# Performance work log

Measured on AMD Instinct MI355X. Metric: run time of the kernel, lower is better.

The kernel has to match this reference:

```python
import jax, jax.numpy as jnp
import numpy as np

B = 4096
N_FEAT = 4
VOCAB = 100000
EMB = 64
N_NEG = 3
TEMP = 1.0
EPS = 1e-8  # torch.cosine_similarity eps


def setup_inputs() -> dict:
    key = jax.random.key(0)
    ks = jax.random.split(key, 12)
    inp = {}
    inp['user_ids'] = jax.random.randint(ks[0], (B, N_FEAT), 0, VOCAB)
    inp['item_ids'] = jax.random.randint(ks[1], (B, N_FEAT), 0, VOCAB)
    inp['sw_ids'] = jax.random.randint(ks[2], (B,), 0, VOCAB)
    inp['user_tables'] = jax.random.normal(ks[3], (N_FEAT, VOCAB, EMB), jnp.float32) * 0.05
    inp['item_tables'] = jax.random.normal(ks[4], (N_FEAT, VOCAB, EMB), jnp.float32) * 0.05
    # sample weights must be positive (log is taken)
    inp['sw_table'] = jax.random.uniform(ks[5], (VOCAB,), jnp.float32) * 0.99 + 0.01
    inp['uW1'] = jax.random.normal(ks[6], (256, 256), jnp.float32) * 0.05
    inp['ub1'] = jnp.zeros((256,), jnp.float32)
    inp['uW2'] = jax.random.normal(ks[7], (256, 128), jnp.float32) * 0.05
    inp['ub2'] = jnp.zeros((128,), jnp.float32)
    inp['iW1'] = jax.random.normal(ks[8], (256, 256), jnp.float32) * 0.05
    inp['ib1'] = jnp.zeros((256,), jnp.float32)
    inp['iW2'] = jax.random.normal(ks[9], (256, 128), jnp.float32) * 0.05
    inp['ib2'] = jnp.zeros((128,), jnp.float32)
    return inp


def _embed(tables, ids):
    # tables: [F, V, E], ids: [B, F] -> [B, F*E]
    e = jax.vmap(lambda tbl, idx: tbl[idx], in_axes=(0, 1))(tables, ids)  # [F, B, E]
    return jnp.transpose(e, (1, 0, 2)).reshape(ids.shape[0], -1)


def _mlp(x, W1, b1, W2, b2):
    # torch-rechub MLP with output_layer=False: activation after every layer
    h = jax.nn.relu(x @ W1 + b1)
    return jax.nn.relu(h @ W2 + b2)


def reference(user_ids, item_ids, sw_ids, user_tables, item_tables, sw_table,
              uW1, ub1, uW2, ub2, iW1, ib1, iW2, ib2):
    u = _mlp(_embed(user_tables, user_ids), uW1, ub1, uW2, ub2)   # [B, 128]
    v = _mlp(_embed(item_tables, item_ids), iW1, ib1, iW2, ib2)   # [B, 128]
    un = u / jnp.maximum(jnp.linalg.norm(u, axis=-1, keepdims=True), EPS)
    vn = v / jnp.maximum(jnp.linalg.norm(v, axis=-1, keepdims=True), EPS)
    pred = un @ vn.T                                              # [B, B] cosine sim
    sw = sw_table[sw_ids]                                         # [B]
    scores = pred - jnp.log(sw)[None, :]                          # debias per item column
    # in-batch negative sampling: row i pairs with cols (i..i+n_neg) mod B
    rows = jnp.repeat(jnp.arange(B), N_NEG + 1)
    cols = ((jnp.arange(B)[:, None] + jnp.arange(N_NEG + 1)[None, :]) % B).reshape(-1)
    out = scores[rows, cols] / TEMP
    return out.reshape(B, N_NEG + 1)
```

## Files before the change

### kernel.cpp

```cpp
#include <hip/hip_runtime.h>
#include <math.h>

#define BATCH 4096
#define NFEAT 4
#define VOCAB 100000
#define EMB 64
#define D_IN 256
#define D_H 256
#define D_O 128
#define ROWS 16
#define XS_STRIDE 264
#define YS_STRIDE 132

typedef __attribute__((ext_vector_type(8))) short bf16x8;
typedef __attribute__((ext_vector_type(4))) float f32x4;

__device__ inline ushort f2bf(float f) {
  union { float f; unsigned u; } v; v.f = f;
  unsigned u = v.u;
  return (ushort)((u + 0x7fffu + ((u >> 16) & 1u)) >> 16);
}

__global__ __launch_bounds__(256) void prep_kernel(
    const float* __restrict__ uW1, const float* __restrict__ uW2,
    const float* __restrict__ iW1, const float* __restrict__ iW2,
    ushort* __restrict__ W1tu, ushort* __restrict__ W2tu,
    ushort* __restrict__ W1ti, ushort* __restrict__ W2ti) {
  int idx = blockIdx.x * 256 + threadIdx.x;
  if (idx < 65536) {
    int n = idx >> 8, k = idx & 255;
    W1tu[idx] = f2bf(uW1[k * 256 + n]);
  } else if (idx < 131072) {
    int j = idx - 65536; int n = j >> 8, k = j & 255;
    W1ti[j] = f2bf(iW1[k * 256 + n]);
  } else if (idx < 163840) {
    int j = idx - 131072; int n = j >> 8, k = j & 255;
    W2tu[j] = f2bf(uW2[k * 128 + n]);
  } else {
    int j = idx - 163840; int n = j >> 8, k = j & 255;
    W2ti[j] = f2bf(iW2[k * 128 + n]);
  }
}

__global__ __launch_bounds__(256) void tower_kernel(
    const int* __restrict__ user_ids, const int* __restrict__ item_ids,
    const float* __restrict__ user_tables, const float* __restrict__ item_tables,
    const ushort* __restrict__ W1tu, const float* __restrict__ ub1,
    const ushort* __restrict__ W2tu, const float* __restrict__ ub2,
    const ushort* __restrict__ W1ti, const float* __restrict__ ib1,
    const ushort* __restrict__ W2ti, const float* __restrict__ ib2,
    float* __restrict__ U, float* __restrict__ V) {
  const int tower = blockIdx.y;
  const int* ids = tower ? item_ids : user_ids;
  const float* tab = tower ? item_tables : user_tables;
  const ushort* W1t = tower ? W1ti : W1tu;
  const float* b1 = tower ? ib1 : ub1;
  const ushort* W2t = tower ? W2ti : W2tu;
  const float* b2 = tower ? ib2 : ub2;
  float* O = tower ? V : U;

  const int r0 = blockIdx.x * ROWS;
  const int tid = threadIdx.x;

  __shared__ ushort Xs[ROWS][XS_STRIDE];
  __shared__ ushort Hs[ROWS][XS_STRIDE];
  __shared__ float Ys[ROWS][YS_STRIDE];

#pragma unroll
  for (int i = 0; i < 4; i++) {
    int slot = i * 256 + tid;
    int row = slot >> 6;
    int c4 = slot & 63;
    int f = c4 >> 4;
    int id = ids[(size_t)(r0 + row) * NFEAT + f];
    float4 v = ((const float4*)(tab + ((size_t)f * VOCAB + (size_t)id) * EMB))[c4 & 15];
    ushort4 o = {f2bf(v.x), f2bf(v.y), f2bf(v.z), f2bf(v.w)};
    *(ushort4*)&Xs[row][c4 * 4] = o;
  }
  __syncthreads();

  const int lane = tid & 63;
  const int w = tid >> 6;
  const int m = lane & 15;
  const int quad = lane >> 4;

  {
    bf16x8 a[8];
#pragma unroll
    for (int k0 = 0; k0 < 8; k0++)
      a[k0] = *(const bf16x8*)&Xs[m][k0 * 32 + quad * 8];
#pragma unroll
    for (int ct = 0; ct < 4; ct++) {
      int n = (w * 4 + ct) * 16 + m;
      const ushort* wp = W1t + (size_t)n * 256 + quad * 8;
      f32x4 acc = {0.f, 0.f, 0.f, 0.f};
#pragma unroll
      for (int k0 = 0; k0 < 8; k0++)
        acc = __builtin_amdgcn_mfma_f32_16x16x32_bf16(
            a[k0], *(const bf16x8*)(wp + k0 * 32), acc, 0, 0, 0);
      float bias = b1[n];
#pragma unroll
      for (int reg = 0; reg < 4; reg++) {
        int r = quad * 4 + reg;
        Hs[r][n] = f2bf(fmaxf(acc[reg] + bias, 0.f));
      }
    }
  }
  __syncthreads();

  {
    bf16x8 h[8];
#pragma unroll
    for (int k0 = 0; k0 < 8; k0++)
      h[k0] = *(const bf16x8*)&Hs[m][k0 * 32 + quad * 8];
#pragma unroll
    for (int ct = 0; ct < 2; ct++) {
      int n = (w * 2 + ct) * 16 + m;
      const ushort* wp = W2t + (size_t)n * 256 + quad * 8;
      f32x4 acc = {0.f, 0.f, 0.f, 0.f};
#pragma unroll
      for (int k0 = 0; k0 < 8; k0++)
        acc = __builtin_amdgcn_mfma_f32_16x16x32_bf16(
            h[k0], *(const bf16x8*)(wp + k0 * 32), acc, 0, 0, 0);
      float bias = b2[n];
#pragma unroll
      for (int reg = 0; reg < 4; reg++) {
        int r = quad * 4 + reg;
        Ys[r][n] = fmaxf(acc[reg] + bias, 0.f);
      }
    }
  }
  __syncthreads();

#pragma unroll
  for (int rr = 0; rr < 4; rr++) {
    int row = w * 4 + rr;
    float y0 = Ys[row][lane];
    float y1 = Ys[row][64 + lane];
    float s = y0 * y0 + y1 * y1;
#pragma unroll
    for (int off = 32; off; off >>= 1) s += __shfl_xor(s, off);
    float inv = 1.f / fmaxf(sqrtf(s), 1e-8f);
    float* op = O + (size_t)(r0 + row) * D_O;
    op[lane] = y0 * inv;
    op[64 + lane] = y1 * inv;
  }
}

__global__ __launch_bounds__(256) void score_kernel(
    const float* __restrict__ U, const float* __restrict__ V,
    const int* __restrict__ sw_ids, const float* __restrict__ sw_table,
    float* __restrict__ out) {
  int wave = threadIdx.x >> 6;
  int lane = threadIdx.x & 63;
  int i = blockIdx.x * 4 + wave;

  float u0 = U[(size_t)i * D_O + lane];
  float u1 = U[(size_t)i * D_O + 64 + lane];

#pragma unroll
  for (int j = 0; j < 4; j++) {
    int c = (i + j) & (BATCH - 1);
    float v0 = V[(size_t)c * D_O + lane];
    float v1 = V[(size_t)c * D_O + 64 + lane];
    float d = u0 * v0 + u1 * v1;
#pragma unroll
    for (int off = 32; off; off >>= 1) d += __shfl_xor(d, off);
    if (lane == 0) {
      out[(size_t)i * 4 + j] = d - logf(sw_table[sw_ids[c]]);
    }
  }
}

extern "C" void kernel_launch(void* const* d_in, const int* in_sizes, int n_in,
                              void* d_out, int out_size, void* d_ws, size_t ws_size,
                              hipStream_t stream) {
  (void)in_sizes; (void)n_in; (void)out_size; (void)ws_size;
  const int*   user_ids    = (const int*)d_in[0];
  const int*   item_ids    = (const int*)d_in[1];
  const int*   sw_ids      = (const int*)d_in[2];
  const float* user_tables = (const float*)d_in[3];
  const float* item_tables = (const float*)d_in[4];
  const float* sw_table    = (const float*)d_in[5];
  const float* uW1 = (const float*)d_in[6];
  const float* ub1 = (const float*)d_in[7];
  const float* uW2 = (const float*)d_in[8];
  const float* ub2 = (const float*)d_in[9];
  const float* iW1 = (const float*)d_in[10];
  const float* ib1 = (const float*)d_in[11];
  const float* iW2 = (const float*)d_in[12];
  const float* ib2 = (const float*)d_in[13];
  float* out = (float*)d_out;

  float* U = (float*)d_ws;
  float* V = U + (size_t)BATCH * D_O;
  ushort* W1tu = (ushort*)(V + (size_t)BATCH * D_O);
  ushort* W1ti = W1tu + 256 * 256;
  ushort* W2tu = W1ti + 256 * 256;
  ushort* W2ti = W2tu + 128 * 256;

  prep_kernel<<<768, 256, 0, stream>>>(uW1, uW2, iW1, iW2, W1tu, W2tu, W1ti, W2ti);

  tower_kernel<<<dim3(BATCH / ROWS, 2), 256, 0, stream>>>(
      user_ids, item_ids, user_tables, item_tables,
      W1tu, ub1, W2tu, ub2, W1ti, ib1, W2ti, ib2, U, V);

  score_kernel<<<BATCH / 4, 256, 0, stream>>>(U, V, sw_ids, sw_table, out);
}
```

Before: 217.7 us.

## Fuse tower MLPs and score computation into one kernel with halo item rows

Merges the two-tower MLP kernel and the score kernel into one. Each block embeds and runs both MLPs for its 16 user rows plus 19 item rows (3 halo rows, padded to 48 MFMA rows), normalizes them in shared memory, and computes the four debiased scores locally. This removes the U/V round trip through global memory and one kernel launch. The cost is redundant halo item computation, zero-padded MFMA rows, and half as many blocks, each doing more serial work.

```diff
diff --git a/kernel.cpp b/kernel.cpp
--- a/kernel.cpp
+++ b/kernel.cpp
@@ -5,12 +5,12 @@
 #define NFEAT 4
 #define VOCAB 100000
 #define EMB 64
-#define D_IN 256
-#define D_H 256
 #define D_O 128
 #define ROWS 16
+#define TROWS 48
+#define LIVE_ROWS 35
 #define XS_STRIDE 264
-#define YS_STRIDE 132
+#define YS_F_STRIDE 132
 
 typedef __attribute__((ext_vector_type(8))) short bf16x8;
 typedef __attribute__((ext_vector_type(4))) float f32x4;
@@ -42,53 +42,66 @@
   }
 }
 
-__global__ __launch_bounds__(256) void tower_kernel(
+__global__ __launch_bounds__(256) void fused_kernel(
     const int* __restrict__ user_ids, const int* __restrict__ item_ids,
+    const int* __restrict__ sw_ids,
     const float* __restrict__ user_tables, const float* __restrict__ item_tables,
+    const float* __restrict__ sw_table,
     const ushort* __restrict__ W1tu, const float* __restrict__ ub1,
     const ushort* __restrict__ W2tu, const float* __restrict__ ub2,
     const ushort* __restrict__ W1ti, const float* __restrict__ ib1,
     const ushort* __restrict__ W2ti, const float* __restrict__ ib2,
-    float* __restrict__ U, float* __restrict__ V) {
-  const int tower = blockIdx.y;
-  const int* ids = tower ? item_ids : user_ids;
-  const float* tab = tower ? item_tables : user_tables;
-  const ushort* W1t = tower ? W1ti : W1tu;
-  const float* b1 = tower ? ib1 : ub1;
-  const ushort* W2t = tower ? W2ti : W2tu;
-  const float* b2 = tower ? ib2 : ub2;
-  float* O = tower ? V : U;
-
+    float* __restrict__ out) {
   const int r0 = blockIdx.x * ROWS;
   const int tid = threadIdx.x;
-
-  __shared__ ushort Xs[ROWS][XS_STRIDE];
-  __shared__ ushort Hs[ROWS][XS_STRIDE];
-  __shared__ float Ys[ROWS][YS_STRIDE];
-
-#pragma unroll
-  for (int i = 0; i < 4; i++) {
-    int slot = i * 256 + tid;
-    int row = slot >> 6;
-    int c4 = slot & 63;
-    int f = c4 >> 4;
-    int id = ids[(size_t)(r0 + row) * NFEAT + f];
-    float4 v = ((const float4*)(tab + ((size_t)f * VOCAB + (size_t)id) * EMB))[c4 & 15];
-    ushort4 o = {f2bf(v.x), f2bf(v.y), f2bf(v.z), f2bf(v.w)};
-    *(ushort4*)&Xs[row][c4 * 4] = o;
-  }
-  __syncthreads();
-
   const int lane = tid & 63;
   const int w = tid >> 6;
   const int m = lane & 15;
   const int quad = lane >> 4;
 
-  {
+  __shared__ __align__(16) char XsRaw[TROWS * XS_STRIDE * 2];
+  __shared__ ushort Hs[TROWS][XS_STRIDE];
+  __shared__ float Lsw[32];
+  ushort* Xs = (ushort*)XsRaw;
+  float* Yf = (float*)XsRaw;
+
+  if (tid < 19) {
+    int c = (r0 + tid) & (BATCH - 1);
+    Lsw[tid] = logf(sw_table[sw_ids[c]]);
+  }
+
+#pragma unroll
+  for (int i = 0; i < 9; i++) {
+    int slot = i * 256 + tid;
+    if (slot < LIVE_ROWS * 64) {
+      int row = slot >> 6;
+      int c4 = slot & 63;
+      int f = c4 >> 4;
+      const int* ids = (row < ROWS) ? user_ids : item_ids;
+      const float* tab = (row < ROWS) ? user_tables : item_tables;
+      int grow = (row < ROWS) ? (r0 + row) : ((r0 + row - ROWS) & (BATCH - 1));
+      int id = ids[grow * NFEAT + f];
+      float4 v = ((const float4*)(tab + ((size_t)f * VOCAB + (size_t)id) * EMB))[c4 & 15];
+      ushort4 o = {f2bf(v.x), f2bf(v.y), f2bf(v.z), f2bf(v.w)};
+      *(ushort4*)&Xs[row * XS_STRIDE + c4 * 4] = o;
+    }
+  }
+  for (int s = LIVE_ROWS * 64 + tid; s < TROWS * 64; s += 256) {
+    int row = s >> 6;
+    int c4 = s & 63;
+    ushort4 z = {0, 0, 0, 0};
+    *(ushort4*)&Xs[row * XS_STRIDE + c4 * 4] = z;
+  }
+  __syncthreads();
+
+#pragma unroll
+  for (int mt = 0; mt < 3; mt++) {
+    const ushort* W1t = mt ? W1ti : W1tu;
+    const float* b1 = mt ? ib1 : ub1;
     bf16x8 a[8];
 #pragma unroll
     for (int k0 = 0; k0 < 8; k0++)
-      a[k0] = *(const bf16x8*)&Xs[m][k0 * 32 + quad * 8];
+      a[k0] = *(const bf16x8*)&Xs[(mt * 16 + m) * XS_STRIDE + k0 * 32 + quad * 8];
 #pragma unroll
     for (int ct = 0; ct < 4; ct++) {
       int n = (w * 4 + ct) * 16 + m;
@@ -100,19 +113,20 @@
             a[k0], *(const bf16x8*)(wp + k0 * 32), acc, 0, 0, 0);
       float bias = b1[n];
 #pragma unroll
-      for (int reg = 0; reg < 4; reg++) {
-        int r = quad * 4 + reg;
-        Hs[r][n] = f2bf(fmaxf(acc[reg] + bias, 0.f));
-      }
-    }
-  }
-  __syncthreads();
-
-  {
+      for (int reg = 0; reg < 4; reg++)
+        Hs[mt * 16 + quad * 4 + reg][n] = f2bf(fmaxf(acc[reg] + bias, 0.f));
+    }
+  }
+  __syncthreads();
+
+#pragma unroll
+  for (int mt = 0; mt < 3; mt++) {
+    const ushort* W2t = mt ? W2ti : W2tu;
+    const float* b2 = mt ? ib2 : ub2;
     bf16x8 h[8];
 #pragma unroll
     for (int k0 = 0; k0 < 8; k0++)
-      h[k0] = *(const bf16x8*)&Hs[m][k0 * 32 + quad * 8];
+      h[k0] = *(const bf16x8*)&Hs[mt * 16 + m][k0 * 32 + quad * 8];
 #pragma unroll
     for (int ct = 0; ct < 2; ct++) {
       int n = (w * 2 + ct) * 16 + m;
@@ -124,50 +138,41 @@
             h[k0], *(const bf16x8*)(wp + k0 * 32), acc, 0, 0, 0);
       float bias = b2[n];
 #pragma unroll
-      for (int reg = 0; reg < 4; reg++) {
-        int r = quad * 4 + reg;
-        Ys[r][n] = fmaxf(acc[reg] + bias, 0.f);
-      }
-    }
-  }
-  __syncthreads();
-
-#pragma unroll
-  for (int rr = 0; rr < 4; rr++) {
-    int row = w * 4 + rr;
-    float y0 = Ys[row][lane];
-    float y1 = Ys[row][64 + lane];
+      for (int reg = 0; reg < 4; reg++)
+        Yf[(mt * 16 + quad * 4 + reg) * YS_F_STRIDE + n] =
+            fmaxf(acc[reg] + bias, 0.f);
+    }
+  }
+  __syncthreads();
+
+#pragma unroll
+  for (int rr = 0; rr < 12; rr++) {
+    int row = w * 12 + rr;
+    float y0 = Yf[row * YS_F_STRIDE + lane];
+    float y1 = Yf[row * YS_F_STRIDE + 64 + lane];
     float s = y0 * y0 + y1 * y1;
 #pragma unroll
     for (int off = 32; off; off >>= 1) s += __shfl_xor(s, off);
     float inv = 1.f / fmaxf(sqrtf(s), 1e-8f);
-    float* op = O + (size_t)(r0 + row) * D_O;
-    op[lane] = y0 * inv;
-    op[64 + lane] = y1 * inv;
-  }
-}
-
-__global__ __launch_bounds__(256) void score_kernel(
-    const float* __restrict__ U, const float* __restrict__ V,
-    const int* __restrict__ sw_ids, const float* __restrict__ sw_table,
-    float* __restrict__ out) {
-  int wave = threadIdx.x >> 6;
-  int lane = threadIdx.x & 63;
-  int i = blockIdx.x * 4 + wave;
-
-  float u0 = U[(size_t)i * D_O + lane];
-  float u1 = U[(size_t)i * D_O + 64 + lane];
-
-#pragma unroll
-  for (int j = 0; j < 4; j++) {
-    int c = (i + j) & (BATCH - 1);
-    float v0 = V[(size_t)c * D_O + lane];
-    float v1 = V[(size_t)c * D_O + 64 + lane];
-    float d = u0 * v0 + u1 * v1;
-#pragma unroll
-    for (int off = 32; off; off >>= 1) d += __shfl_xor(d, off);
-    if (lane == 0) {
-      out[(size_t)i * 4 + j] = d - logf(sw_table[sw_ids[c]]);
+    Yf[row * YS_F_STRIDE + lane] = y0 * inv;
+    Yf[row * YS_F_STRIDE + 64 + lane] = y1 * inv;
+  }
+  __syncthreads();
+
+#pragma unroll
+  for (int rr = 0; rr < 4; rr++) {
+    int i = w * 4 + rr;
+    float u0 = Yf[i * YS_F_STRIDE + lane];
+    float u1 = Yf[i * YS_F_STRIDE + 64 + lane];
+#pragma unroll
+    for (int j = 0; j < 4; j++) {
+      int vrow = ROWS + i + j;
+      float v0 = Yf[vrow * YS_F_STRIDE + lane];
+      float v1 = Yf[vrow * YS_F_STRIDE + 64 + lane];
+      float d = u0 * v0 + u1 * v1;
+#pragma unroll
+      for (int off = 32; off; off >>= 1) d += __shfl_xor(d, off);
+      if (lane == 0) out[(size_t)(r0 + i) * 4 + j] = d - Lsw[i + j];
     }
   }
 }
@@ -192,18 +197,14 @@
   const float* ib2 = (const float*)d_in[13];
   float* out = (float*)d_out;
 
-  float* U = (float*)d_ws;
-  float* V = U + (size_t)BATCH * D_O;
-  ushort* W1tu = (ushort*)(V + (size_t)BATCH * D_O);
+  ushort* W1tu = (ushort*)d_ws;
   ushort* W1ti = W1tu + 256 * 256;
   ushort* W2tu = W1ti + 256 * 256;
   ushort* W2ti = W2tu + 128 * 256;
 
   prep_kernel<<<768, 256, 0, stream>>>(uW1, uW2, iW1, iW2, W1tu, W2tu, W1ti, W2ti);
 
-  tower_kernel<<<dim3(BATCH / ROWS, 2), 256, 0, stream>>>(
-      user_ids, item_ids, user_tables, item_tables,
-      W1tu, ub1, W2tu, ub2, W1ti, ib1, W2ti, ib2, U, V);
-
-  score_kernel<<<BATCH / 4, 256, 0, stream>>>(U, V, sw_ids, sw_table, out);
-}
+  fused_kernel<<<dim3(BATCH / ROWS), 256, 0, stream>>>(
+      user_ids, item_ids, sw_ids, user_tables, item_tables, sw_table,
+      W1tu, ub1, W2tu, ub2, W1ti, ib1, W2ti, ib2, out);
+}
```

Result: slower. 232.4 us (+6.8%).
